# Optimization experiments

Measured on AMD Instinct MI355X. Metric: run time of the kernel, lower is better.

Reference implementation:

```python
import jax, jax.numpy as jnp
import numpy as np

M = 128        # max_units (units // 2)
BETA = 15.0

def setup_inputs() -> dict:
    key = jax.random.key(0)
    k1, k2 = jax.random.split(key)
    x = jax.random.normal(k1, (2048, 512), dtype=jnp.float32)
    w = jax.random.normal(k2, (512, 256), dtype=jnp.float32) * 0.05  # 'random_normal' init scale
    return {"x": x, "w": w}

def reference(x, w):
    # s[b, f, u] = beta * (x[b, f] + w[f, u]); shape (B, F, U)
    s = BETA * (x[:, :, None] + w[None, :, :])
    # smooth max over features for first M units
    hv = jax.nn.logsumexp(s[..., :M], axis=1) / BETA          # (B, M)
    # smooth min over features for remaining units
    hw = -jax.nn.logsumexp(-s[..., M:], axis=1) / BETA         # (B, U-M)
    return jnp.concatenate([hv, hw], axis=1)                   # (B, U)
```

## Files before the change

### kernel.cpp

```cpp
#include <hip/hip_runtime.h>

#define B_DIM 2048
#define F_DIM 512
#define U_DIM 256

constexpr float K_L2E = 21.64042561333445f;
constexpr float INV_K = 1.0f / K_L2E;

using short8 = __attribute__((ext_vector_type(8))) short;
using f32x4  = __attribute__((ext_vector_type(4))) float;

__device__ __forceinline__ unsigned short f2bf(float f) {
    unsigned u = __float_as_uint(f);
    return (unsigned short)((u + 0x7FFFu + ((u >> 16) & 1u)) >> 16);
}

__global__ __launch_bounds__(256)
void prep_k(const float* __restrict__ x, const float* __restrict__ w,
            float* __restrict__ mx, float* __restrict__ mn,
            unsigned short* __restrict__ ea, unsigned short* __restrict__ ew) {
    const int tid  = threadIdx.x;
    const int wv   = tid >> 6;
    const int lane = tid & 63;
    const int b    = (blockIdx.x << 2) + wv;

    const float4* xr = reinterpret_cast<const float4*>(x + b * F_DIM);
    float4 v0 = xr[lane * 2];
    float4 v1 = xr[lane * 2 + 1];
    float f8[8] = {v0.x, v0.y, v0.z, v0.w, v1.x, v1.y, v1.z, v1.w};
    float hi = f8[0], lo = f8[0];
#pragma unroll
    for (int i = 1; i < 8; ++i) { hi = fmaxf(hi, f8[i]); lo = fminf(lo, f8[i]); }
#pragma unroll
    for (int off = 32; off; off >>= 1) {
        hi = fmaxf(hi, __shfl_xor(hi, off));
        lo = fminf(lo, __shfl_xor(lo, off));
    }
    if (lane == 0) { mx[b] = hi; mn[b] = lo; }

    const int rt = b >> 4, br = b & 15;
    const int kb = lane >> 2, g = lane & 3;
    const int chunk_lane = br + (g << 4);
    {
        short8 c;
#pragma unroll
        for (int i = 0; i < 8; ++i) c[i] = (short)f2bf(exp2f(K_L2E * (f8[i] - hi)));
        reinterpret_cast<short8*>(ea)[(rt * 16 + kb) * 64 + chunk_lane] = c;
    }
    {
        short8 c;
#pragma unroll
        for (int i = 0; i < 8; ++i) c[i] = (short)f2bf(exp2f(K_L2E * (lo - f8[i])));
        reinterpret_cast<short8*>(ea)[((128 + rt) * 16 + kb) * 64 + chunk_lane] = c;
    }

    if (blockIdx.x < 256) {
        int e  = tid << 1;
        int f  = (blockIdx.x << 1) + (e >> 8);
        int u0 = e & 255;
        float2 wv2 = *reinterpret_cast<const float2*>(w + f * U_DIM + u0);
        const int kbw = f >> 5, gw = (f >> 3) & 3, iw = f & 7;
        float wa[2] = {wv2.x, wv2.y};
#pragma unroll
        for (int j = 0; j < 2; ++j) {
            int u = u0 + j;
            float s = (u < 128) ? K_L2E : -K_L2E;
            int ut = u >> 4;
            int idx = (((ut * 16 + kbw) * 64) + (u & 15) + (gw << 4)) * 8 + iw;
            ew[idx] = f2bf(exp2f(s * wa[j]));
        }
    }
}

__global__ __launch_bounds__(256)
void mfma_k(const unsigned short* __restrict__ ea, const unsigned short* __restrict__ ew,
            const float* __restrict__ mx, const float* __restrict__ mn,
            float* __restrict__ out) {
    const int bid  = blockIdx.x;
    const int rt   = bid >> 2;
    const int utq  = bid & 3;
    const int wv   = threadIdx.x >> 6;
    const int lane = threadIdx.x & 63;
    const int ut   = (utq << 2) + wv;
    const int m    = (ut >= 8);

    const short8* A  = reinterpret_cast<const short8*>(ea) + ((m * 128 + rt) * 16) * 64 + lane;
    const short8* Bp = reinterpret_cast<const short8*>(ew) + (ut * 16) * 64 + lane;

    f32x4 acc = {0.f, 0.f, 0.f, 0.f};
#pragma unroll
    for (int kb = 0; kb < 16; ++kb)
        acc = __builtin_amdgcn_mfma_f32_16x16x32_bf16(A[kb * 64], Bp[kb * 64], acc, 0, 0, 0);

    const int j    = lane & 15;
    const int quad = lane >> 4;
    const float* st = m ? mn : mx;
    const int brow = rt * 16 + (quad << 2);
#pragma unroll
    for (int r = 0; r < 4; ++r) {
        float lg = __log2f(acc[r]) * INV_K;
        float sv = st[brow + r];
        out[(brow + r) * U_DIM + (ut << 4) + j] = m ? (sv - lg) : (sv + lg);
    }
}

extern "C" void kernel_launch(void* const* d_in, const int* in_sizes, int n_in,
                              void* d_out, int out_size, void* d_ws, size_t ws_size,
                              hipStream_t stream) {
    const float* x = (const float*)d_in[0];
    const float* w = (const float*)d_in[1];
    float* out = (float*)d_out;
    float* mx = (float*)d_ws;
    float* mn = mx + B_DIM;
    unsigned short* ea = (unsigned short*)((char*)d_ws + 16384);
    unsigned short* ew = ea + 2 * 128 * 16 * 64 * 8;

    prep_k<<<512, 256, 0, stream>>>(x, w, mx, mn, ea, ew);
    mfma_k<<<512, 256, 0, stream>>>(ea, ew, mx, mn, out);
}
```

Before: 14.41 us.

## Register-block MFMA 2x2 tiles per wave and vectorize packed w-exp writes

The MFMA kernel now has each wave compute a 2x2 block of 16x16 output tiles, reusing each loaded A and B fragment for two MFMAs. This halves global fragment loads per output and cuts the grid to 256 blocks of 128 threads. The w preprocessing now has each thread build a full short8 packed chunk and write it with one vector store, replacing scattered 2-byte writes, though it reads w with a strided gather. Fewer waves (512 versus 2048) may lower latency hiding on a GPU with many CUs.

```diff
diff --git a/kernel.cpp b/kernel.cpp
--- a/kernel.cpp
+++ b/kernel.cpp
@@ -54,53 +54,76 @@
         reinterpret_cast<short8*>(ea)[((128 + rt) * 16 + kb) * 64 + chunk_lane] = c;
     }
 
-    if (blockIdx.x < 256) {
-        int e  = tid << 1;
-        int f  = (blockIdx.x << 1) + (e >> 8);
-        int u0 = e & 255;
-        float2 wv2 = *reinterpret_cast<const float2*>(w + f * U_DIM + u0);
-        const int kbw = f >> 5, gw = (f >> 3) & 3, iw = f & 7;
-        float wa[2] = {wv2.x, wv2.y};
+    if (blockIdx.x < 64) {
+        const int c    = (blockIdx.x << 8) + tid;
+        const int cl   = c & 63;
+        const int ckb  = (c >> 6) & 15;
+        const int cut  = c >> 10;
+        const int u    = (cut << 4) + (cl & 15);
+        const int gw   = cl >> 4;
+        const int fb   = (ckb << 5) + (gw << 3);
+        const float s  = (u < 128) ? K_L2E : -K_L2E;
+        short8 cc;
 #pragma unroll
-        for (int j = 0; j < 2; ++j) {
-            int u = u0 + j;
-            float s = (u < 128) ? K_L2E : -K_L2E;
-            int ut = u >> 4;
-            int idx = (((ut * 16 + kbw) * 64) + (u & 15) + (gw << 4)) * 8 + iw;
-            ew[idx] = f2bf(exp2f(s * wa[j]));
-        }
+        for (int i = 0; i < 8; ++i)
+            cc[i] = (short)f2bf(exp2f(s * w[(fb + i) * U_DIM + u]));
+        reinterpret_cast<short8*>(ew)[c] = cc;
     }
 }
 
-__global__ __launch_bounds__(256)
+__global__ __launch_bounds__(128)
 void mfma_k(const unsigned short* __restrict__ ea, const unsigned short* __restrict__ ew,
             const float* __restrict__ mx, const float* __restrict__ mn,
             float* __restrict__ out) {
-    const int bid  = blockIdx.x;
-    const int rt   = bid >> 2;
-    const int utq  = bid & 3;
     const int wv   = threadIdx.x >> 6;
     const int lane = threadIdx.x & 63;
-    const int ut   = (utq << 2) + wv;
-    const int m    = (ut >= 8);
+    const int gid  = (blockIdx.x << 1) + wv;
+    const int rtp  = gid >> 3;
+    const int utp  = gid & 7;
+    const int rt0  = rtp << 1;
+    const int ut0  = utp << 1;
+    const int m    = (utp >= 4);
 
-    const short8* A  = reinterpret_cast<const short8*>(ea) + ((m * 128 + rt) * 16) * 64 + lane;
-    const short8* Bp = reinterpret_cast<const short8*>(ew) + (ut * 16) * 64 + lane;
+    const short8* A0 = reinterpret_cast<const short8*>(ea) + ((m * 128 + rt0) * 16) * 64 + lane;
+    const short8* A1 = A0 + 16 * 64;
+    const short8* B0 = reinterpret_cast<const short8*>(ew) + (ut0 * 16) * 64 + lane;
+    const short8* B1 = B0 + 16 * 64;
 
-    f32x4 acc = {0.f, 0.f, 0.f, 0.f};
+    f32x4 acc00 = {0.f,0.f,0.f,0.f}, acc01 = {0.f,0.f,0.f,0.f};
+    f32x4 acc10 = {0.f,0.f,0.f,0.f}, acc11 = {0.f,0.f,0.f,0.f};
 #pragma unroll
-    for (int kb = 0; kb < 16; ++kb)
-        acc = __builtin_amdgcn_mfma_f32_16x16x32_bf16(A[kb * 64], Bp[kb * 64], acc, 0, 0, 0);
+    for (int kb = 0; kb < 16; ++kb) {
+        short8 a0 = A0[kb * 64];
+        short8 a1 = A1[kb * 64];
+        short8 b0 = B0[kb * 64];
+        short8 b1 = B1[kb * 64];
+        acc00 = __builtin_amdgcn_mfma_f32_16x16x32_bf16(a0, b0, acc00, 0, 0, 0);
+        acc01 = __builtin_amdgcn_mfma_f32_16x16x32_bf16(a0, b1, acc01, 0, 0, 0);
+        acc10 = __builtin_amdgcn_mfma_f32_16x16x32_bf16(a1, b0, acc10, 0, 0, 0);
+        acc11 = __builtin_amdgcn_mfma_f32_16x16x32_bf16(a1, b1, acc11, 0, 0, 0);
+    }
 
     const int j    = lane & 15;
     const int quad = lane >> 4;
     const float* st = m ? mn : mx;
-    const int brow = rt * 16 + (quad << 2);
+
 #pragma unroll
-    for (int r = 0; r < 4; ++r) {
-        float lg = __log2f(acc[r]) * INV_K;
-        float sv = st[brow + r];
-        out[(brow + r) * U_DIM + (ut << 4) + j] = m ? (sv - lg) : (sv + lg);
+    for (int ri = 0; ri < 2; ++ri) {
+        const int brow = (rt0 + ri) * 16 + (quad << 2);
+#pragma unroll
+        for (int r = 0; r < 4; ++r) {
+            float sv = st[brow + r];
+            {
+                f32x4 a = ri ? acc10 : acc00;
+                float lg = __log2f(a[r]) * INV_K;
+                out[(brow + r) * U_DIM + (ut0 << 4) + j] = m ? (sv - lg) : (sv + lg);
+            }
+            {
+                f32x4 a = ri ? acc11 : acc01;
+                float lg = __log2f(a[r]) * INV_K;
+                out[(brow + r) * U_DIM + ((ut0 + 1) << 4) + j] = m ? (sv - lg) : (sv + lg);
+            }
+        }
     }
 }
 
@@ -116,5 +139,5 @@
     unsigned short* ew = ea + 2 * 128 * 16 * 64 * 8;
 
     prep_k<<<512, 256, 0, stream>>>(x, w, mx, mn, ea, ew);
-    mfma_k<<<512, 256, 0, stream>>>(ea, ew, mx, mn, out);
+    mfma_k<<<256, 128, 0, stream>>>(ea, ew, mx, mn, out);
 }
```

After: 16.11 us. 11.8% more time.

## Fuse x-side exp prep into MFMA kernel via LDS, split w prep

Applied to the files above, without the earlier changes.

The x-side max/exp/bf16 packing now happens inside the MFMA kernel: each block computes its 16 rows' shifted exponentials for one mode into swizzled shared memory, then runs the MFMA loop from LDS. The separate global ea buffer and the mx/mn arrays go away, removing a global write and reread. A small dedicated kernel packs w with one 16-byte store per thread. In exchange each x row is read and exponentiated by two blocks per mode, and a block barrier is added.

```diff
diff --git a/kernel.cpp b/kernel.cpp
--- a/kernel.cpp
+++ b/kernel.cpp
@@ -16,91 +16,76 @@
 }
 
 __global__ __launch_bounds__(256)
-void prep_k(const float* __restrict__ x, const float* __restrict__ w,
-            float* __restrict__ mx, float* __restrict__ mn,
-            unsigned short* __restrict__ ea, unsigned short* __restrict__ ew) {
+void prep_w(const float* __restrict__ w, unsigned short* __restrict__ ew) {
+    const int c   = (blockIdx.x << 8) + threadIdx.x;
+    const int cl  = c & 63;
+    const int ckb = (c >> 6) & 15;
+    const int cut = c >> 10;
+    const int u   = (cut << 4) + (cl & 15);
+    const int gw  = cl >> 4;
+    const int fb  = (ckb << 5) + (gw << 3);
+    const float s = (u < 128) ? K_L2E : -K_L2E;
+    short8 cc;
+#pragma unroll
+    for (int i = 0; i < 8; ++i)
+        cc[i] = (short)f2bf(exp2f(s * w[(fb + i) * U_DIM + u]));
+    reinterpret_cast<short8*>(ew)[c] = cc;
+}
+
+__global__ __launch_bounds__(256)
+void fused_k(const float* __restrict__ x, const unsigned short* __restrict__ ew,
+             float* __restrict__ out) {
+    __shared__ short8 sA[1024];
+    __shared__ float  sst[16];
+
     const int tid  = threadIdx.x;
     const int wv   = tid >> 6;
     const int lane = tid & 63;
-    const int b    = (blockIdx.x << 2) + wv;
+    const int rt   = blockIdx.x >> 2;
+    const int utq  = blockIdx.x & 3;
+    const int mode = utq >> 1;
+    const int ut   = (utq << 2) + wv;
 
-    const float4* xr = reinterpret_cast<const float4*>(x + b * F_DIM);
-    float4 v0 = xr[lane * 2];
-    float4 v1 = xr[lane * 2 + 1];
-    float f8[8] = {v0.x, v0.y, v0.z, v0.w, v1.x, v1.y, v1.z, v1.w};
-    float hi = f8[0], lo = f8[0];
+    const int   kb_w = lane >> 2;
+    const int   g_w  = lane & 3;
+    const float sgn  = mode ? -1.f : 1.f;
+
 #pragma unroll
-    for (int i = 1; i < 8; ++i) { hi = fmaxf(hi, f8[i]); lo = fminf(lo, f8[i]); }
+    for (int j = 0; j < 4; ++j) {
+        const int row = (wv << 2) + j;
+        const float4* xr = reinterpret_cast<const float4*>(x + (rt * 16 + row) * F_DIM);
+        float4 v0 = xr[lane * 2];
+        float4 v1 = xr[lane * 2 + 1];
+        float t[8] = {sgn * v0.x, sgn * v0.y, sgn * v0.z, sgn * v0.w,
+                      sgn * v1.x, sgn * v1.y, sgn * v1.z, sgn * v1.w};
+        float hi = t[0];
 #pragma unroll
-    for (int off = 32; off; off >>= 1) {
-        hi = fmaxf(hi, __shfl_xor(hi, off));
-        lo = fminf(lo, __shfl_xor(lo, off));
+        for (int i = 1; i < 8; ++i) hi = fmaxf(hi, t[i]);
+#pragma unroll
+        for (int off = 32; off; off >>= 1) hi = fmaxf(hi, __shfl_xor(hi, off));
+        if (lane == 0) sst[row] = hi;
+        short8 cb;
+#pragma unroll
+        for (int i = 0; i < 8; ++i) cb[i] = (short)f2bf(exp2f(K_L2E * (t[i] - hi)));
+        sA[(kb_w << 6) + ((row + (g_w << 4)) ^ (kb_w & 7))] = cb;
     }
-    if (lane == 0) { mx[b] = hi; mn[b] = lo; }
+    __syncthreads();
 
-    const int rt = b >> 4, br = b & 15;
-    const int kb = lane >> 2, g = lane & 3;
-    const int chunk_lane = br + (g << 4);
-    {
-        short8 c;
-#pragma unroll
-        for (int i = 0; i < 8; ++i) c[i] = (short)f2bf(exp2f(K_L2E * (f8[i] - hi)));
-        reinterpret_cast<short8*>(ea)[(rt * 16 + kb) * 64 + chunk_lane] = c;
-    }
-    {
-        short8 c;
-#pragma unroll
-        for (int i = 0; i < 8; ++i) c[i] = (short)f2bf(exp2f(K_L2E * (lo - f8[i])));
-        reinterpret_cast<short8*>(ea)[((128 + rt) * 16 + kb) * 64 + chunk_lane] = c;
-    }
-
-    if (blockIdx.x < 256) {
-        int e  = tid << 1;
-        int f  = (blockIdx.x << 1) + (e >> 8);
-        int u0 = e & 255;
-        float2 wv2 = *reinterpret_cast<const float2*>(w + f * U_DIM + u0);
-        const int kbw = f >> 5, gw = (f >> 3) & 3, iw = f & 7;
-        float wa[2] = {wv2.x, wv2.y};
-#pragma unroll
-        for (int j = 0; j < 2; ++j) {
-            int u = u0 + j;
-            float s = (u < 128) ? K_L2E : -K_L2E;
-            int ut = u >> 4;
-            int idx = (((ut * 16 + kbw) * 64) + (u & 15) + (gw << 4)) * 8 + iw;
-            ew[idx] = f2bf(exp2f(s * wa[j]));
-        }
-    }
-}
-
-__global__ __launch_bounds__(256)
-void mfma_k(const unsigned short* __restrict__ ea, const unsigned short* __restrict__ ew,
-            const float* __restrict__ mx, const float* __restrict__ mn,
-            float* __restrict__ out) {
-    const int bid  = blockIdx.x;
-    const int rt   = bid >> 2;
-    const int utq  = bid & 3;
-    const int wv   = threadIdx.x >> 6;
-    const int lane = threadIdx.x & 63;
-    const int ut   = (utq << 2) + wv;
-    const int m    = (ut >= 8);
-
-    const short8* A  = reinterpret_cast<const short8*>(ea) + ((m * 128 + rt) * 16) * 64 + lane;
-    const short8* Bp = reinterpret_cast<const short8*>(ew) + (ut * 16) * 64 + lane;
-
+    const short8* B = reinterpret_cast<const short8*>(ew) + (ut << 4) * 64 + lane;
     f32x4 acc = {0.f, 0.f, 0.f, 0.f};
 #pragma unroll
-    for (int kb = 0; kb < 16; ++kb)
-        acc = __builtin_amdgcn_mfma_f32_16x16x32_bf16(A[kb * 64], Bp[kb * 64], acc, 0, 0, 0);
+    for (int kb = 0; kb < 16; ++kb) {
+        short8 a = sA[(kb << 6) + (lane ^ (kb & 7))];
+        acc = __builtin_amdgcn_mfma_f32_16x16x32_bf16(a, B[kb * 64], acc, 0, 0, 0);
+    }
 
     const int j    = lane & 15;
     const int quad = lane >> 4;
-    const float* st = m ? mn : mx;
-    const int brow = rt * 16 + (quad << 2);
 #pragma unroll
     for (int r = 0; r < 4; ++r) {
-        float lg = __log2f(acc[r]) * INV_K;
-        float sv = st[brow + r];
-        out[(brow + r) * U_DIM + (ut << 4) + j] = m ? (sv - lg) : (sv + lg);
+        const int row = (quad << 2) + r;
+        float res = sst[row] + __log2f(acc[r]) * INV_K;
+        out[(rt * 16 + row) * U_DIM + (ut << 4) + j] = mode ? -res : res;
     }
 }
 
@@ -110,11 +95,8 @@
     const float* x = (const float*)d_in[0];
     const float* w = (const float*)d_in[1];
     float* out = (float*)d_out;
-    float* mx = (float*)d_ws;
-    float* mn = mx + B_DIM;
-    unsigned short* ea = (unsigned short*)((char*)d_ws + 16384);
-    unsigned short* ew = ea + 2 * 128 * 16 * 64 * 8;
+    unsigned short* ew = (unsigned short*)d_ws;
 
-    prep_k<<<512, 256, 0, stream>>>(x, w, mx, mn, ea, ew);
-    mfma_k<<<512, 256, 0, stream>>>(ea, ew, mx, mn, out);
+    prep_w<<<64, 256, 0, stream>>>(w, ew);
+    fused_k<<<512, 256, 0, stream>>>(x, ew, out);
 }
```

After: 14.96 us. 3.8% more time.
